# Kernel optimization log

Measured on AMD Instinct MI355X. Metric: run time of the kernel, lower is better.

Reference implementation:

```python
import jax, jax.numpy as jnp
import numpy as np

NUM_HEADS = 4
KERNEL = 7


def setup_inputs() -> dict:
    key = jax.random.key(0)
    k = jax.random.split(key, 6)
    B, H, W, C = 4, 64, 64, 128
    kk = KERNEL
    x = jax.random.normal(k[0], (B, H, W, C), dtype=jnp.float32)
    w_qkv = jax.random.normal(k[1], (C, 3 * C), dtype=jnp.float32) * 0.02
    b_qkv = jnp.zeros((3 * C,), dtype=jnp.float32)
    rpb = jax.random.normal(k[2], (NUM_HEADS, 2 * kk - 1, 2 * kk - 1), dtype=jnp.float32) * 0.02
    w_proj = jax.random.normal(k[3], (C, C), dtype=jnp.float32) * 0.02
    b_proj = jnp.zeros((C,), dtype=jnp.float32)
    return {"x": x, "w_qkv": w_qkv, "b_qkv": b_qkv, "rpb": rpb,
            "w_proj": w_proj, "b_proj": b_proj}


def reference(x, w_qkv, b_qkv, rpb, w_proj, b_proj):
    B, H, W, C = x.shape
    nh, k = NUM_HEADS, KERNEL
    d = C // nh
    scale = d ** -0.5

    qkv = x @ w_qkv + b_qkv                      # [B,H,W,3C]
    q, kt, v = jnp.split(qkv, 3, axis=-1)
    q = q.reshape(B, H, W, nh, d) * scale
    kt = kt.reshape(B, H, W, nh, d)
    v = v.reshape(B, H, W, nh, d)

    # NATTEN window: centered, clamped at borders (window never shrinks)
    start_h = jnp.clip(jnp.arange(H) - k // 2, 0, H - k)
    start_w = jnp.clip(jnp.arange(W) - k // 2, 0, W - k)
    idx_h = start_h[:, None] + jnp.arange(k)     # [H,k] key rows per query row
    idx_w = start_w[:, None] + jnp.arange(k)     # [W,k]

    kn = kt[:, idx_h][:, :, :, idx_w]            # [B,H,k,W,k,nh,d]
    vn = v[:, idx_h][:, :, :, idx_w]             # [B,H,k,W,k,nh,d]

    scores = jnp.einsum('bxyhd,bxiyjhd->bxyhij', q, kn)  # [B,H,W,nh,k,k]

    # relative position bias: index = (key_pos - query_pos) + (k-1)
    bh = idx_h - jnp.arange(H)[:, None] + (k - 1)        # [H,k] in [0,2k-2]
    bw = idx_w - jnp.arange(W)[:, None] + (k - 1)        # [W,k]
    bias = rpb[:, bh[:, None, :, None], bw[None, :, None, :]]  # [nh,H,W,k,k]
    scores = scores + jnp.transpose(bias, (1, 2, 0, 3, 4))

    attn = jax.nn.softmax(scores.reshape(B, H, W, nh, k * k), axis=-1)
    attn = attn.reshape(B, H, W, nh, k, k)

    out = jnp.einsum('bxyhij,bxiyjhd->bxyhd', attn, vn)  # [B,H,W,nh,d]
    out = out.reshape(B, H, W, C) @ w_proj + b_proj
    return out
```

## Files before the change

kernel.cpp:

```cpp
#include <hip/hip_runtime.h>
#include <cstddef>
#include <cstdint>

#define Hdim 64
#define Wdim 64
#define NH 4
#define DH 32
#define KW 7

typedef _Float16 v2h __attribute__((ext_vector_type(2)));

#if defined(__has_builtin)
#if __has_builtin(__builtin_amdgcn_fdot2)
#define HAVE_FDOT2 1
#endif
#endif

__device__ __forceinline__ float fdot2acc(v2h a, v2h b, float c) {
#ifdef HAVE_FDOT2
    return __builtin_amdgcn_fdot2(a, b, c, false);
#else
    return fmaf((float)a.x, (float)b.x, fmaf((float)a.y, (float)b.y, c));
#endif
}

union F16x8 {
    uint4 u;
    v2h h[4];
};

__global__ __launch_bounds__(256) void gemm_qkv(
    const float* __restrict__ A,
    const float* __restrict__ W,
    const float* __restrict__ bias,
    _Float16* __restrict__ qkvh)
{
    __shared__ float As[32][68];
    __shared__ float Ws[32][132];

    const int m0 = blockIdx.x * 64;
    const int sel = blockIdx.y;
    const int n0 = sel * 128;
    const int tid = threadIdx.x;
    const int tx = tid & 15;
    const int ty = tid >> 4;

    float acc[4][8] = {};

    for (int kc = 0; kc < 128; kc += 32) {
#pragma unroll
        for (int it = 0; it < 2; ++it) {
            int idx = it * 256 + tid;
            int m = idx >> 3;
            int k = (idx & 7) * 4;
            const float4 a = *(const float4*)(A + (size_t)(m0 + m) * 128 + kc + k);
            As[k + 0][m] = a.x; As[k + 1][m] = a.y;
            As[k + 2][m] = a.z; As[k + 3][m] = a.w;
        }
#pragma unroll
        for (int it = 0; it < 4; ++it) {
            int idx = it * 256 + tid;
            int k = idx >> 5;
            int n = (idx & 31) * 4;
            *(float4*)(&Ws[k][n]) = *(const float4*)(W + (size_t)(kc + k) * 384 + n0 + n);
        }
        __syncthreads();

#pragma unroll 8
        for (int k = 0; k < 32; ++k) {
            const float4 a4 = *(const float4*)(&As[k][ty * 4]);
            const float4 b0 = *(const float4*)(&Ws[k][tx * 8]);
            const float4 b1 = *(const float4*)(&Ws[k][tx * 8 + 4]);
            const float a_[4] = {a4.x, a4.y, a4.z, a4.w};
            const float b_[8] = {b0.x, b0.y, b0.z, b0.w, b1.x, b1.y, b1.z, b1.w};
#pragma unroll
            for (int i = 0; i < 4; ++i)
#pragma unroll
                for (int j = 0; j < 8; ++j)
                    acc[i][j] = fmaf(a_[i], b_[j], acc[i][j]);
        }
        __syncthreads();
    }

    const float qscale = (sel == 0) ? 0.17677669529663687f : 1.0f;
    const int h = tx >> 2;
    const int d0 = (tx & 3) * 8;
    float bv[8];
#pragma unroll
    for (int j = 0; j < 8; ++j) bv[j] = bias[n0 + tx * 8 + j];

#pragma unroll
    for (int i = 0; i < 4; ++i) {
        const int m = m0 + ty * 4 + i;
        const int b = m >> 12;
        const int yx = m & 4095;
        _Float16 tmp[8];
#pragma unroll
        for (int j = 0; j < 8; ++j)
            tmp[j] = (_Float16)((acc[i][j] + bv[j]) * qscale);
        _Float16* dst = qkvh + ((size_t)sel * 16 + b * 4 + h) * 131072 + (size_t)yx * 32 + d0;
        *(uint4*)dst = *(const uint4*)tmp;
    }
}

#define ATS 8
#define AMAXPOS 196
#define KST 40

__global__ __launch_bounds__(256, 4) void local_attn(
    const _Float16* __restrict__ qkvh,
    const float* __restrict__ rpb,
    float* __restrict__ outp)
{
    __shared__ _Float16 kS[AMAXPOS * KST];
    __shared__ _Float16 vS[AMAXPOS * KST];
    __shared__ float rS[169];

    const int bh = blockIdx.x;
    const int h = bh & 3;
    const int ty0 = blockIdx.y * ATS;
    const int tx0 = blockIdx.z * ATS;
    const int tid = threadIdx.x;

    const int lo_h = max(0, min(ty0 - 3, Hdim - KW));
    const int hi_h = min(ty0 + ATS - 4, Hdim - KW) + KW - 1;
    const int lo_w = max(0, min(tx0 - 3, Wdim - KW));
    const int hi_w = min(tx0 + ATS - 4, Wdim - KW) + KW - 1;
    const int ch = hi_h - lo_h + 1;
    const int cw = hi_w - lo_w + 1;
    const int npos = ch * cw;

    const _Float16* kbase = qkvh + (size_t)(16 + bh) * 131072;
    const _Float16* vbase = qkvh + (size_t)(32 + bh) * 131072;

    for (int idx = tid; idx < npos * 4; idx += 256) {
        const int pos = idx >> 2;
        const int c = idx & 3;
        const int ry = pos / cw;
        const int rx = pos - ry * cw;
        const size_t g = ((size_t)(lo_h + ry) * Wdim + (lo_w + rx)) * 32 + c * 8;
        *(uint4*)(kS + pos * KST + c * 8) = *(const uint4*)(kbase + g);
        *(uint4*)(vS + pos * KST + c * 8) = *(const uint4*)(vbase + g);
    }
    for (int i = tid; i < 169; i += 256) rS[i] = rpb[h * 169 + i];
    __syncthreads();

    const int p = tid >> 2;
    const int q = tid & 3;
    const int py = p >> 3, px = p & 7;
    const int y = ty0 + py, x = tx0 + px;
    const int sh = max(0, min(y - 3, Hdim - KW));
    const int sw = max(0, min(x - 3, Wdim - KW));
    const int rb = sh - lo_h;
    const int cb = sw - lo_w;
    const int bh0 = sh - y + 6;
    const int bw0 = sw - x + 6;

    F16x8 qf;
    qf.u = *(const uint4*)(qkvh + (size_t)bh * 131072 + ((size_t)y * Wdim + x) * 32 + q * 8);

    float sc[49];
#pragma unroll
    for (int i = 0; i < KW; ++i) {
        const _Float16* kp = kS + ((rb + i) * cw + cb) * KST + q * 8;
        const int bi = (bh0 + i) * 13 + bw0;
#pragma unroll
        for (int j = 0; j < KW; ++j) {
            F16x8 kf;
            kf.u = *(const uint4*)(kp + j * KST);
            float s = fdot2acc(qf.h[0], kf.h[0],
                      fdot2acc(qf.h[1], kf.h[1],
                      fdot2acc(qf.h[2], kf.h[2],
                      fdot2acc(qf.h[3], kf.h[3], 0.0f))));
            s += __shfl_xor(s, 1);
            s += __shfl_xor(s, 2);
            sc[i * KW + j] = s + rS[bi + j];
        }
    }

    float mx = sc[0];
#pragma unroll
    for (int t = 1; t < 49; ++t) mx = fmaxf(mx, sc[t]);
    float l = 0.f;
#pragma unroll
    for (int t = 0; t < 49; ++t) { sc[t] = __expf(sc[t] - mx); l += sc[t]; }
    const float inv = 1.f / l;

    float o[8] = {};
#pragma unroll
    for (int i = 0; i < KW; ++i) {
        const _Float16* vp = vS + ((rb + i) * cw + cb) * KST + q * 8;
#pragma unroll
        for (int j = 0; j < KW; ++j) {
            F16x8 vf;
            vf.u = *(const uint4*)(vp + j * KST);
            const float w = sc[i * KW + j] * inv;
#pragma unroll
            for (int d = 0; d < 4; ++d) {
                o[2 * d + 0] = fmaf(w, (float)vf.h[d].x, o[2 * d + 0]);
                o[2 * d + 1] = fmaf(w, (float)vf.h[d].y, o[2 * d + 1]);
            }
        }
    }

    const size_t pix = (size_t)(bh >> 2) * 4096 + (size_t)y * Wdim + x;
    float* dst = outp + pix * 128 + h * DH + q * 8;
    *(float4*)(dst)     = make_float4(o[0], o[1], o[2], o[3]);
    *(float4*)(dst + 4) = make_float4(o[4], o[5], o[6], o[7]);
}

__global__ __launch_bounds__(256) void gemm_proj(
    const float* __restrict__ A,
    const float* __restrict__ W,
    const float* __restrict__ bias,
    float* __restrict__ C)
{
    __shared__ float As[32][68];
    __shared__ float Ws[32][64];

    const int m0 = blockIdx.x * 64;
    const int n0 = blockIdx.y * 64;
    const int tid = threadIdx.x;
    const int tx = tid & 15;
    const int ty = tid >> 4;

    float acc[4][4] = {};

    for (int kc = 0; kc < 128; kc += 32) {
#pragma unroll
        for (int it = 0; it < 2; ++it) {
            int idx = it * 256 + tid;
            int m = idx >> 3;
            int k = (idx & 7) * 4;
            const float4 a = *(const float4*)(A + (size_t)(m0 + m) * 128 + kc + k);
            As[k + 0][m] = a.x; As[k + 1][m] = a.y;
            As[k + 2][m] = a.z; As[k + 3][m] = a.w;
        }
#pragma unroll
        for (int it = 0; it < 2; ++it) {
            int idx = it * 256 + tid;
            int k = idx >> 4;
            int n = (idx & 15) * 4;
            *(float4*)(&Ws[k][n]) = *(const float4*)(W + (size_t)(kc + k) * 128 + n0 + n);
        }
        __syncthreads();

#pragma unroll 8
        for (int k = 0; k < 32; ++k) {
            const float4 a4 = *(const float4*)(&As[k][ty * 4]);
            const float4 b4 = *(const float4*)(&Ws[k][tx * 4]);
            const float a_[4] = {a4.x, a4.y, a4.z, a4.w};
            const float b_[4] = {b4.x, b4.y, b4.z, b4.w};
#pragma unroll
            for (int i = 0; i < 4; ++i)
#pragma unroll
                for (int j = 0; j < 4; ++j)
                    acc[i][j] = fmaf(a_[i], b_[j], acc[i][j]);
        }
        __syncthreads();
    }

    const float4 bia = *(const float4*)(bias + n0 + tx * 4);
#pragma unroll
    for (int i = 0; i < 4; ++i) {
        const size_t m = (size_t)(m0 + ty * 4 + i);
        float4 r;
        r.x = acc[i][0] + bia.x;
        r.y = acc[i][1] + bia.y;
        r.z = acc[i][2] + bia.z;
        r.w = acc[i][3] + bia.w;
        *(float4*)(C + m * 128 + n0 + tx * 4) = r;
    }
}

extern "C" void kernel_launch(void* const* d_in, const int* in_sizes, int n_in,
                              void* d_out, int out_size, void* d_ws, size_t ws_size,
                              hipStream_t stream) {
    const float* x      = (const float*)d_in[0];
    const float* w_qkv  = (const float*)d_in[1];
    const float* b_qkv  = (const float*)d_in[2];
    const float* rpb    = (const float*)d_in[3];
    const float* w_proj = (const float*)d_in[4];
    const float* b_proj = (const float*)d_in[5];
    float* out = (float*)d_out;

    _Float16* qkvh = (_Float16*)d_ws;
    float* attnb = (float*)((char*)d_ws + 3ULL * 16 * 4096 * 32 * 2);

    dim3 blk(256);
    gemm_qkv<<<dim3(16384 / 64, 3), blk, 0, stream>>>(x, w_qkv, b_qkv, qkvh);
    local_attn<<<dim3(16, Hdim / ATS, Wdim / ATS), blk, 0, stream>>>(qkvh, rpb, attnb);
    gemm_proj<<<dim3(16384 / 64, 2), blk, 0, stream>>>(attnb, w_proj, b_proj, out);
}
```

Baseline: 125.2 us.

## Use fp16 MFMA for QKV and projection GEMMs with transposed fp16 weights

Replaces both fp32 FMA-based GEMMs with MFMA 16x16x32 fp16 matrix-core kernels. A new prep kernel transposes and converts both weight matrices to fp16 on each call. The attention output is now written as fp16, halving that intermediate's traffic. This trades fp32 accuracy for fp16 inputs and adds one small launch. Epilogue stores are now scalar and poorly coalesced.

```diff
diff --git a/kernel.cpp b/kernel.cpp
--- a/kernel.cpp
+++ b/kernel.cpp
@@ -7,8 +7,11 @@
 #define NH 4
 #define DH 32
 #define KW 7
+#define QSCALE 0.17677669529663687f
 
 typedef _Float16 v2h __attribute__((ext_vector_type(2)));
+typedef _Float16 half8 __attribute__((ext_vector_type(8)));
+typedef float f32x4 __attribute__((ext_vector_type(4)));
 
 #if defined(__has_builtin)
 #if __has_builtin(__builtin_amdgcn_fdot2)
@@ -29,77 +32,91 @@
     v2h h[4];
 };
 
-__global__ __launch_bounds__(256) void gemm_qkv(
+__global__ __launch_bounds__(256) void prep_weights(
+    const float* __restrict__ wq, const float* __restrict__ wp,
+    _Float16* __restrict__ wqT, _Float16* __restrict__ wpT)
+{
+    __shared__ float Ts[64][65];
+    int blk = blockIdx.x;
+    const float* src;
+    _Float16* dst;
+    int N, kt, nt;
+    if (blk < 12) { src = wq; dst = wqT; N = 384; kt = blk / 6; nt = blk % 6; }
+    else { blk -= 12; src = wp; dst = wpT; N = 128; kt = blk >> 1; nt = blk & 1; }
+    const int k0 = kt * 64, n0 = nt * 64;
+    const int tid = threadIdx.x;
+
+#pragma unroll
+    for (int it = 0; it < 16; ++it) {
+        int idx = it * 256 + tid;
+        int r = idx >> 6, c = idx & 63;
+        Ts[r][c] = src[(size_t)(k0 + r) * N + n0 + c];
+    }
+    __syncthreads();
+#pragma unroll
+    for (int it = 0; it < 2; ++it) {
+        int idx = it * 256 + tid;
+        int n = idx >> 3;
+        int kq = (idx & 7) * 8;
+        _Float16 tmp[8];
+#pragma unroll
+        for (int j = 0; j < 8; ++j) tmp[j] = (_Float16)Ts[kq + j][n];
+        *(uint4*)(dst + (size_t)(n0 + n) * 128 + k0 + kq) = *(const uint4*)tmp;
+    }
+}
+
+__global__ __launch_bounds__(256) void gemm_qkv_mfma(
     const float* __restrict__ A,
-    const float* __restrict__ W,
+    const _Float16* __restrict__ WT,
     const float* __restrict__ bias,
     _Float16* __restrict__ qkvh)
 {
-    __shared__ float As[32][68];
-    __shared__ float Ws[32][132];
-
+    __shared__ _Float16 As[64 * 136];
     const int m0 = blockIdx.x * 64;
     const int sel = blockIdx.y;
     const int n0 = sel * 128;
     const int tid = threadIdx.x;
-    const int tx = tid & 15;
-    const int ty = tid >> 4;
-
-    float acc[4][8] = {};
-
-    for (int kc = 0; kc < 128; kc += 32) {
-#pragma unroll
-        for (int it = 0; it < 2; ++it) {
-            int idx = it * 256 + tid;
-            int m = idx >> 3;
-            int k = (idx & 7) * 4;
-            const float4 a = *(const float4*)(A + (size_t)(m0 + m) * 128 + kc + k);
-            As[k + 0][m] = a.x; As[k + 1][m] = a.y;
-            As[k + 2][m] = a.z; As[k + 3][m] = a.w;
-        }
-#pragma unroll
-        for (int it = 0; it < 4; ++it) {
-            int idx = it * 256 + tid;
-            int k = idx >> 5;
-            int n = (idx & 31) * 4;
-            *(float4*)(&Ws[k][n]) = *(const float4*)(W + (size_t)(kc + k) * 384 + n0 + n);
-        }
-        __syncthreads();
-
-#pragma unroll 8
-        for (int k = 0; k < 32; ++k) {
-            const float4 a4 = *(const float4*)(&As[k][ty * 4]);
-            const float4 b0 = *(const float4*)(&Ws[k][tx * 8]);
-            const float4 b1 = *(const float4*)(&Ws[k][tx * 8 + 4]);
-            const float a_[4] = {a4.x, a4.y, a4.z, a4.w};
-            const float b_[8] = {b0.x, b0.y, b0.z, b0.w, b1.x, b1.y, b1.z, b1.w};
-#pragma unroll
-            for (int i = 0; i < 4; ++i)
-#pragma unroll
-                for (int j = 0; j < 8; ++j)
-                    acc[i][j] = fmaf(a_[i], b_[j], acc[i][j]);
-        }
-        __syncthreads();
-    }
-
-    const float qscale = (sel == 0) ? 0.17677669529663687f : 1.0f;
-    const int h = tx >> 2;
-    const int d0 = (tx & 3) * 8;
-    float bv[8];
-#pragma unroll
-    for (int j = 0; j < 8; ++j) bv[j] = bias[n0 + tx * 8 + j];
-
-#pragma unroll
-    for (int i = 0; i < 4; ++i) {
-        const int m = m0 + ty * 4 + i;
-        const int b = m >> 12;
-        const int yx = m & 4095;
-        _Float16 tmp[8];
-#pragma unroll
-        for (int j = 0; j < 8; ++j)
-            tmp[j] = (_Float16)((acc[i][j] + bv[j]) * qscale);
-        _Float16* dst = qkvh + ((size_t)sel * 16 + b * 4 + h) * 131072 + (size_t)yx * 32 + d0;
-        *(uint4*)dst = *(const uint4*)tmp;
+    const int wv = tid >> 6;
+    const int ln = tid & 15;
+    const int quad = (tid & 63) >> 4;
+
+#pragma unroll
+    for (int it = 0; it < 8; ++it) {
+        int idx = it * 256 + tid;
+        int m = idx >> 5;
+        int kq = (idx & 31) * 4;
+        float4 a = *(const float4*)(A + (size_t)(m0 + m) * 128 + kq);
+        _Float16 t[4] = {(_Float16)a.x, (_Float16)a.y, (_Float16)a.z, (_Float16)a.w};
+        *(uint2*)(As + m * 136 + kq) = *(const uint2*)t;
+    }
+    __syncthreads();
+
+    f32x4 acc[8] = {};
+    const int mrow = wv * 16 + ln;
+#pragma unroll
+    for (int ks = 0; ks < 4; ++ks) {
+        const half8 af = *(const half8*)(As + mrow * 136 + ks * 32 + quad * 8);
+#pragma unroll
+        for (int nt = 0; nt < 8; ++nt) {
+            const half8 bf = *(const half8*)(WT + (size_t)(n0 + nt * 16 + ln) * 128 + ks * 32 + quad * 8);
+            acc[nt] = __builtin_amdgcn_mfma_f32_16x16x32_f16(af, bf, acc[nt], 0, 0, 0);
+        }
+    }
+
+    const float qscale = (sel == 0) ? QSCALE : 1.0f;
+#pragma unroll
+    for (int nt = 0; nt < 8; ++nt) {
+        const int n = n0 + nt * 16 + ln;
+        const float bv = bias[n];
+        const int h = (n >> 5) & 3;
+        const int d = n & 31;
+#pragma unroll
+        for (int r = 0; r < 4; ++r) {
+            const int m = m0 + wv * 16 + quad * 4 + r;
+            const int b = m >> 12, yx = m & 4095;
+            qkvh[((size_t)sel * 16 + b * 4 + h) * 131072 + (size_t)yx * 32 + d] =
+                (_Float16)((acc[nt][r] + bv) * qscale);
+        }
     }
 }
 
@@ -110,7 +127,7 @@
 __global__ __launch_bounds__(256, 4) void local_attn(
     const _Float16* __restrict__ qkvh,
     const float* __restrict__ rpb,
-    float* __restrict__ outp)
+    _Float16* __restrict__ outh)
 {
     __shared__ _Float16 kS[AMAXPOS * KST];
     __shared__ _Float16 vS[AMAXPOS * KST];
@@ -204,72 +221,55 @@
     }
 
     const size_t pix = (size_t)(bh >> 2) * 4096 + (size_t)y * Wdim + x;
-    float* dst = outp + pix * 128 + h * DH + q * 8;
-    *(float4*)(dst)     = make_float4(o[0], o[1], o[2], o[3]);
-    *(float4*)(dst + 4) = make_float4(o[4], o[5], o[6], o[7]);
-}
-
-__global__ __launch_bounds__(256) void gemm_proj(
-    const float* __restrict__ A,
-    const float* __restrict__ W,
+    _Float16 oh[8];
+#pragma unroll
+    for (int d = 0; d < 8; ++d) oh[d] = (_Float16)o[d];
+    *(uint4*)(outh + pix * 128 + h * DH + q * 8) = *(const uint4*)oh;
+}
+
+__global__ __launch_bounds__(256) void gemm_proj_mfma(
+    const _Float16* __restrict__ Ah,
+    const _Float16* __restrict__ WT,
     const float* __restrict__ bias,
     float* __restrict__ C)
 {
-    __shared__ float As[32][68];
-    __shared__ float Ws[32][64];
-
+    __shared__ _Float16 As[64 * 136];
     const int m0 = blockIdx.x * 64;
-    const int n0 = blockIdx.y * 64;
-    const int tid = threadIdx.x;
-    const int tx = tid & 15;
-    const int ty = tid >> 4;
-
-    float acc[4][4] = {};
-
-    for (int kc = 0; kc < 128; kc += 32) {
-#pragma unroll
-        for (int it = 0; it < 2; ++it) {
-            int idx = it * 256 + tid;
-            int m = idx >> 3;
-            int k = (idx & 7) * 4;
-            const float4 a = *(const float4*)(A + (size_t)(m0 + m) * 128 + kc + k);
-            As[k + 0][m] = a.x; As[k + 1][m] = a.y;
-            As[k + 2][m] = a.z; As[k + 3][m] = a.w;
-        }
-#pragma unroll
-        for (int it = 0; it < 2; ++it) {
-            int idx = it * 256 + tid;
-            int k = idx >> 4;
-            int n = (idx & 15) * 4;
-            *(float4*)(&Ws[k][n]) = *(const float4*)(W + (size_t)(kc + k) * 128 + n0 + n);
-        }
-        __syncthreads();
-
-#pragma unroll 8
-        for (int k = 0; k < 32; ++k) {
-            const float4 a4 = *(const float4*)(&As[k][ty * 4]);
-            const float4 b4 = *(const float4*)(&Ws[k][tx * 4]);
-            const float a_[4] = {a4.x, a4.y, a4.z, a4.w};
-            const float b_[4] = {b4.x, b4.y, b4.z, b4.w};
-#pragma unroll
-            for (int i = 0; i < 4; ++i)
-#pragma unroll
-                for (int j = 0; j < 4; ++j)
-                    acc[i][j] = fmaf(a_[i], b_[j], acc[i][j]);
-        }
-        __syncthreads();
-    }
-
-    const float4 bia = *(const float4*)(bias + n0 + tx * 4);
-#pragma unroll
-    for (int i = 0; i < 4; ++i) {
-        const size_t m = (size_t)(m0 + ty * 4 + i);
-        float4 r;
-        r.x = acc[i][0] + bia.x;
-        r.y = acc[i][1] + bia.y;
-        r.z = acc[i][2] + bia.z;
-        r.w = acc[i][3] + bia.w;
-        *(float4*)(C + m * 128 + n0 + tx * 4) = r;
+    const int tid = threadIdx.x;
+    const int wv = tid >> 6;
+    const int ln = tid & 15;
+    const int quad = (tid & 63) >> 4;
+
+#pragma unroll
+    for (int it = 0; it < 4; ++it) {
+        int idx = it * 256 + tid;
+        int m = idx >> 4;
+        int kq = (idx & 15) * 8;
+        *(uint4*)(As + m * 136 + kq) = *(const uint4*)(Ah + (size_t)(m0 + m) * 128 + kq);
+    }
+    __syncthreads();
+
+    f32x4 acc[8] = {};
+    const int mrow = wv * 16 + ln;
+#pragma unroll
+    for (int ks = 0; ks < 4; ++ks) {
+        const half8 af = *(const half8*)(As + mrow * 136 + ks * 32 + quad * 8);
+#pragma unroll
+        for (int nt = 0; nt < 8; ++nt) {
+            const half8 bf = *(const half8*)(WT + (size_t)(nt * 16 + ln) * 128 + ks * 32 + quad * 8);
+            acc[nt] = __builtin_amdgcn_mfma_f32_16x16x32_f16(af, bf, acc[nt], 0, 0, 0);
+        }
+    }
+
+#pragma unroll
+    for (int nt = 0; nt < 8; ++nt) {
+        const int n = nt * 16 + ln;
+        const float bv = bias[n];
+#pragma unroll
+        for (int r = 0; r < 4; ++r) {
+            const int m = m0 + wv * 16 + quad * 4 + r;
+            C[(size_t)m * 128 + n] = acc[nt][r] + bv;
+        }
     }
 }
 
@@ -284,11 +284,15 @@
     const float* b_proj = (const float*)d_in[5];
     float* out = (float*)d_out;
 
-    _Float16* qkvh = (_Float16*)d_ws;
-    float* attnb = (float*)((char*)d_ws + 3ULL * 16 * 4096 * 32 * 2);
+    char* ws = (char*)d_ws;
+    _Float16* qkvh = (_Float16*)ws;
+    _Float16* attnh = (_Float16*)(ws + 12582912);
+    _Float16* wqT = (_Float16*)(ws + 12582912 + 4194304);
+    _Float16* wpT = (_Float16*)(ws + 12582912 + 4194304 + 98304);
 
     dim3 blk(256);
-    gemm_qkv<<<dim3(16384 / 64, 3), blk, 0, stream>>>(x, w_qkv, b_qkv, qkvh);
-    local_attn<<<dim3(16, Hdim / ATS, Wdim / ATS), blk, 0, stream>>>(qkvh, rpb, attnb);
-    gemm_proj<<<dim3(16384 / 64, 2), blk, 0, stream>>>(attnb, w_proj, b_proj, out);
-}
+    prep_weights<<<16, blk, 0, stream>>>(w_qkv, w_proj, wqT, wpT);
+    gemm_qkv_mfma<<<dim3(16384 / 64, 3), blk, 0, stream>>>(x, wqT, b_qkv, qkvh);
+    local_attn<<<dim3(16, Hdim / ATS, Wdim / ATS), blk, 0, stream>>>(qkvh, rpb, attnh);
+    gemm_proj_mfma<<<dim3(16384 / 64, 1), blk, 0, stream>>>(attnh, wpT, b_proj, out);
+}
```

After: 239.3 us. 1.91x slower.
